# Optimization experiments

Measured on AMD Instinct MI355X. Metric: run time of the kernel, lower is better.

The kernel has to match this reference:

```python
import jax, jax.numpy as jnp
import numpy as np

NUM_ITEMS = 50000
IN_FEATS = 64
H_FEATS = 64
NUM_EDGES = 800000


def setup_inputs() -> dict:
    key = jax.random.key(0)
    ks = jax.random.split(key, 12)
    s_in = 1.0 / np.sqrt(IN_FEATS)
    s_h = 1.0 / np.sqrt(H_FEATS)
    return {
        "embed": jax.random.normal(ks[0], (NUM_ITEMS, IN_FEATS), jnp.float32),
        "W1_self": jax.random.normal(ks[1], (IN_FEATS, H_FEATS), jnp.float32) * s_in,
        "W1_neigh": jax.random.normal(ks[2], (IN_FEATS, H_FEATS), jnp.float32) * s_in,
        "b1": jax.random.normal(ks[3], (H_FEATS,), jnp.float32) * s_in,
        "W2_self": jax.random.normal(ks[4], (H_FEATS, H_FEATS), jnp.float32) * s_h,
        "W2_neigh": jax.random.normal(ks[5], (H_FEATS, H_FEATS), jnp.float32) * s_h,
        "b2": jax.random.normal(ks[6], (H_FEATS,), jnp.float32) * s_h,
        "W_fc": jax.random.normal(ks[7], (H_FEATS, IN_FEATS), jnp.float32) * s_h,
        "b_fc": jax.random.normal(ks[8], (IN_FEATS,), jnp.float32) * s_h,
        "item_ids": jnp.arange(NUM_ITEMS, dtype=jnp.int64),
        "src": jax.random.randint(ks[9], (NUM_EDGES,), 0, NUM_ITEMS, jnp.int64),
        "dst": jax.random.randint(ks[10], (NUM_EDGES,), 0, NUM_ITEMS, jnp.int64),
    }


def _sage_mean(h, src, dst, W_self, W_neigh, b, num_nodes):
    # gather src features along edges, mean-reduce into dst nodes
    agg = jax.ops.segment_sum(h[src], dst, num_segments=num_nodes)  # [N, d]
    deg = jax.ops.segment_sum(jnp.ones_like(dst, dtype=h.dtype), dst,
                              num_segments=num_nodes)
    h_neigh = agg / jnp.clip(deg, 1.0, None)[:, None]  # zero for isolated nodes
    return h @ W_self + h_neigh @ W_neigh + b


def reference(embed, W1_self, W1_neigh, b1, W2_self, W2_neigh, b2,
              W_fc, b_fc, item_ids, src, dst):
    n = embed.shape[0]
    x = embed[item_ids]                                   # embedding lookup [N, in]
    h = _sage_mean(x, src, dst, W1_self, W1_neigh, b1, n)  # SAGEConv 1
    h = jax.nn.relu(h)
    h = _sage_mean(h, src, dst, W2_self, W2_neigh, b2, n)  # SAGEConv 2
    return h @ W_fc + b_fc                                 # final linear
```

## Files before the change

### kernel.cpp

```cpp
#include <hip/hip_runtime.h>

#define NN 50000
#define NE 800000
#define F  64
#define CAP 64
#define NTILE 782
#define TPB   512

typedef float f32x4 __attribute__((ext_vector_type(4)));
typedef float f32x2 __attribute__((ext_vector_type(2)));

__device__ __forceinline__ unsigned bf16rne(float f) {
    unsigned u = __float_as_uint(f);
    return (u + 0x7fffu + ((u >> 16) & 1u)) >> 16;
}
__device__ __forceinline__ float bflo(unsigned p) { return __uint_as_float(p << 16); }
__device__ __forceinline__ float bfhi(unsigned p) { return __uint_as_float(p & 0xffff0000u); }
__device__ __forceinline__ f32x2 up2(unsigned p) {
    f32x2 r;
    r.x = __uint_as_float(p << 16);
    r.y = __uint_as_float(p & 0xffff0000u);
    return r;
}

__device__ __forceinline__ int nswz(int f, int n) { return f * 64 + (n ^ (((f >> 3) & 3) << 3)); }
__device__ __forceinline__ int aswz(int r, int n) { return r * 64 + (n ^ (((r >> 2) & 3) << 3)); }

__device__ __forceinline__ void add8(f32x2 s[4], const uint4 v) {
    s[0] += up2(v.x);
    s[1] += up2(v.y);
    s[2] += up2(v.z);
    s[3] += up2(v.w);
}


__launch_bounds__(256)
__global__ void k_build(const int* __restrict__ src, const int* __restrict__ dst,
                        int* __restrict__ cnt, unsigned short* __restrict__ csr,
                        const float* __restrict__ embed, const int* __restrict__ ids,
                        uint2* __restrict__ xb) {
    const int t = blockIdx.x * blockDim.x + threadIdx.x;
    if (t >= NE / 4) return;

    const int e0 = t * 4;
    const int4 d4 = *(const int4*)&dst[e0];
    const int4 s4 = *(const int4*)&src[e0];
    int sl0 = atomicAdd(&cnt[d4.x], 1) & (CAP - 1);
    int sl1 = atomicAdd(&cnt[d4.y], 1) & (CAP - 1);
    int sl2 = atomicAdd(&cnt[d4.z], 1) & (CAP - 1);
    int sl3 = atomicAdd(&cnt[d4.w], 1) & (CAP - 1);
    __builtin_nontemporal_store((unsigned short)s4.x, &csr[d4.x * CAP + sl0]);
    __builtin_nontemporal_store((unsigned short)s4.y, &csr[d4.y * CAP + sl1]);
    __builtin_nontemporal_store((unsigned short)s4.z, &csr[d4.z * CAP + sl2]);
    __builtin_nontemporal_store((unsigned short)s4.w, &csr[d4.w * CAP + sl3]);

    const int i  = t >> 2;
    const int c0 = (t & 3) * 4;
    const int rb = ids[i] * 16 + c0;
    float4 v0 = ((const float4*)embed)[rb + 0];
    float4 v1 = ((const float4*)embed)[rb + 1];
    float4 v2 = ((const float4*)embed)[rb + 2];
    float4 v3 = ((const float4*)embed)[rb + 3];
    uint4 p01, p23;
    p01.x = bf16rne(v0.x) | (bf16rne(v0.y) << 16);
    p01.y = bf16rne(v0.z) | (bf16rne(v0.w) << 16);
    p01.z = bf16rne(v1.x) | (bf16rne(v1.y) << 16);
    p01.w = bf16rne(v1.z) | (bf16rne(v1.w) << 16);
    p23.x = bf16rne(v2.x) | (bf16rne(v2.y) << 16);
    p23.y = bf16rne(v2.z) | (bf16rne(v2.w) << 16);
    p23.z = bf16rne(v3.x) | (bf16rne(v3.y) << 16);
    p23.w = bf16rne(v3.z) | (bf16rne(v3.w) << 16);
    uint4* xo = (uint4*)&xb[i * 16 + c0];
    xo[0] = p01;
    xo[1] = p23;
}


template <bool LAST>
__launch_bounds__(TPB)
__global__ void k_fused(const uint4* __restrict__ Ab, const int* __restrict__ cnt,
                        const unsigned short* __restrict__ csr,
                        const float* __restrict__ Ws, const float* __restrict__ Wn,
                        const float* __restrict__ b,
                        const float* __restrict__ Wfc, const float* __restrict__ bfc,
                        uint2* __restrict__ outb, float* __restrict__ out) {
    __shared__ alignas(16) float    NsT[F * 64];
    __shared__ alignas(16) unsigned Apk[32 * 64];
    __shared__ alignas(16) unsigned Wpk[F * F];

    const int tid = threadIdx.x;
    const int node0 = blockIdx.x * 64;

    for (int i = tid; i < F * F; i += TPB)
        Wpk[i] = bf16rne(Ws[i]) | (bf16rne(Wn[i]) << 16);

    {
        const int n = tid >> 3;
        const int c = tid & 7;
        const int lane = tid & 63;
        const int base = lane & 56;
        const int gnode = node0 + n;
        f32x2 s[4];
        s[0] = 0.f; s[1] = 0.f; s[2] = 0.f; s[3] = 0.f;
        uint4 a = make_uint4(0u, 0u, 0u, 0u);
        float inv = 0.f;
        if (gnode < NN) {
            a = Ab[gnode * 8 + c];
            int dc = cnt[gnode];
            int deg = dc < CAP ? dc : CAP;
            const int beg = gnode * CAP;
            int j = 0;
            for (; j + 8 <= deg; j += 8) {
                int v = (int)csr[beg + j + c];
                int i0 = __shfl(v, base + 0, 64), i1 = __shfl(v, base + 1, 64);
                int i2 = __shfl(v, base + 2, 64), i3 = __shfl(v, base + 3, 64);
                int i4 = __shfl(v, base + 4, 64), i5 = __shfl(v, base + 5, 64);
                int i6 = __shfl(v, base + 6, 64), i7 = __shfl(v, base + 7, 64);
                uint4 d0 = Ab[i0 * 8 + c], d1 = Ab[i1 * 8 + c];
                uint4 d2 = Ab[i2 * 8 + c], d3 = Ab[i3 * 8 + c];
                uint4 d4 = Ab[i4 * 8 + c], d5 = Ab[i5 * 8 + c];
                uint4 d6 = Ab[i6 * 8 + c], d7 = Ab[i7 * 8 + c];
                add8(s, d0); add8(s, d1); add8(s, d2); add8(s, d3);
                add8(s, d4); add8(s, d5); add8(s, d6); add8(s, d7);
            }
            int rem = deg - j;
            if (rem > 0) {
                int v = (int)csr[beg + j + (c < rem ? c : 0)];
                int idx[8];
#pragma unroll
                for (int k = 0; k < 8; ++k) idx[k] = __shfl(v, base + k, 64);
#pragma unroll
                for (int k = 0; k < 8; ++k)
                    if (k < rem) { uint4 d = Ab[idx[k] * 8 + c]; add8(s, d); }
            }
            inv = (deg > 0) ? 1.f / (float)deg : 0.f;
        }
        const int f = 8 * c;
        Apk[aswz(4 * c + 0, n)] = a.x;
        Apk[aswz(4 * c + 1, n)] = a.y;
        Apk[aswz(4 * c + 2, n)] = a.z;
        Apk[aswz(4 * c + 3, n)] = a.w;
#pragma unroll
        for (int q = 0; q < 4; ++q) {
            NsT[nswz(f + 2 * q + 0, n)] = s[q].x * inv;
            NsT[nswz(f + 2 * q + 1, n)] = s[q].y * inv;
        }
    }
    __syncthreads();

    const int tx = tid & 15, ty = tid >> 4;
    f32x2 acc[2][2];
    {
        f32x2 b01, b23;
        b01.x = b[4 * tx + 0]; b01.y = b[4 * tx + 1];
        b23.x = b[4 * tx + 2]; b23.y = b[4 * tx + 3];
        acc[0][0] = b01; acc[0][1] = b23;
        acc[1][0] = b01; acc[1][1] = b23;
    }
#pragma unroll 4
    for (int r = 0; r < 32; ++r) {
        const int k0 = 2 * r;
        uint2  ap = *(const uint2*)&Apk[aswz(r, 2 * ty)];
        float2 n0 = *(const float2*)&NsT[nswz(k0, 2 * ty)];
        float2 n1 = *(const float2*)&NsT[nswz(k0 + 1, 2 * ty)];
        uint4  w0 = *(const uint4*)&Wpk[k0 * 64 + 4 * tx];
        uint4  w1 = *(const uint4*)&Wpk[(k0 + 1) * 64 + 4 * tx];
        f32x2 ws0A, ws0B, wn0A, wn0B, ws1A, ws1B, wn1A, wn1B;
        ws0A.x = bflo(w0.x); ws0A.y = bflo(w0.y); ws0B.x = bflo(w0.z); ws0B.y = bflo(w0.w);
        wn0A.x = bfhi(w0.x); wn0A.y = bfhi(w0.y); wn0B.x = bfhi(w0.z); wn0B.y = bfhi(w0.w);
        ws1A.x = bflo(w1.x); ws1A.y = bflo(w1.y); ws1B.x = bflo(w1.z); ws1B.y = bflo(w1.w);
        wn1A.x = bfhi(w1.x); wn1A.y = bfhi(w1.y); wn1B.x = bfhi(w1.z); wn1B.y = bfhi(w1.w);
        const float a00 = bflo(ap.x), a01 = bfhi(ap.x);
        const float a10 = bflo(ap.y), a11 = bfhi(ap.y);
        acc[0][0] += a00 * ws0A + n0.x * wn0A;
        acc[0][1] += a00 * ws0B + n0.x * wn0B;
        acc[1][0] += a10 * ws0A + n0.y * wn0A;
        acc[1][1] += a10 * ws0B + n0.y * wn0B;
        acc[0][0] += a01 * ws1A + n1.x * wn1A;
        acc[0][1] += a01 * ws1B + n1.x * wn1B;
        acc[1][0] += a11 * ws1A + n1.y * wn1A;
        acc[1][1] += a11 * ws1B + n1.y * wn1B;
    }

    if (!LAST) {
#pragma unroll
        for (int i = 0; i < 2; ++i) {
            int node = node0 + 2 * ty + i;
            if (node < NN) {
                float o0 = acc[i][0].x > 0.f ? acc[i][0].x : 0.f;
                float o1 = acc[i][0].y > 0.f ? acc[i][0].y : 0.f;
                float o2 = acc[i][1].x > 0.f ? acc[i][1].x : 0.f;
                float o3 = acc[i][1].y > 0.f ? acc[i][1].y : 0.f;
                uint2 p;
                p.x = bf16rne(o0) | (bf16rne(o1) << 16);
                p.y = bf16rne(o2) | (bf16rne(o3) << 16);
                outb[node * 16 + tx] = p;
            }
        }
    } else {
        __syncthreads();
        float* Wf = (float*)Wpk;
#pragma unroll
        for (int i = 0; i < 2; ++i) {
            NsT[nswz(4 * tx + 0, 2 * ty + i)] = acc[i][0].x;
            NsT[nswz(4 * tx + 1, 2 * ty + i)] = acc[i][0].y;
            NsT[nswz(4 * tx + 2, 2 * ty + i)] = acc[i][1].x;
            NsT[nswz(4 * tx + 3, 2 * ty + i)] = acc[i][1].y;
        }
        for (int i = tid; i < F * F / 4; i += TPB)
            ((float4*)Wf)[i] = ((const float4*)Wfc)[i];
        __syncthreads();

        f32x2 acc2[2][2];
        {
            f32x2 b01, b23;
            b01.x = bfc[4 * tx + 0]; b01.y = bfc[4 * tx + 1];
            b23.x = bfc[4 * tx + 2]; b23.y = bfc[4 * tx + 3];
            acc2[0][0] = b01; acc2[0][1] = b23;
            acc2[1][0] = b01; acc2[1][1] = b23;
        }
#pragma unroll 4
        for (int k = 0; k < 64; ++k) {
            float2 a2 = *(const float2*)&NsT[nswz(k, 2 * ty)];
            float4 w4 = *(const float4*)&Wf[k * 64 + 4 * tx];
            f32x2 wA, wB;
            wA.x = w4.x; wA.y = w4.y; wB.x = w4.z; wB.y = w4.w;
            acc2[0][0] += a2.x * wA; acc2[0][1] += a2.x * wB;
            acc2[1][0] += a2.y * wA; acc2[1][1] += a2.y * wB;
        }
#pragma unroll
        for (int i = 0; i < 2; ++i) {
            int node = node0 + 2 * ty + i;
            if (node < NN) {
                f32x4 o;
                o.x = acc2[i][0].x; o.y = acc2[i][0].y;
                o.z = acc2[i][1].x; o.w = acc2[i][1].y;
                __builtin_nontemporal_store(o, (f32x4*)&out[node * 64 + 4 * tx]);
            }
        }
    }
}


extern "C" void kernel_launch(void* const* d_in, const int* in_sizes, int n_in,
                              void* d_out, int out_size, void* d_ws, size_t ws_size,
                              hipStream_t stream) {
    const float* embed = (const float*)d_in[0];
    const float* W1s = (const float*)d_in[1];
    const float* W1n = (const float*)d_in[2];
    const float* b1  = (const float*)d_in[3];
    const float* W2s = (const float*)d_in[4];
    const float* W2n = (const float*)d_in[5];
    const float* b2  = (const float*)d_in[6];
    const float* Wfc = (const float*)d_in[7];
    const float* bfc = (const float*)d_in[8];
    const int* ids = (const int*)d_in[9];
    const int* src = (const int*)d_in[10];
    const int* dst = (const int*)d_in[11];
    float* out = (float*)d_out;

    char* ws = (char*)d_ws;
    size_t off = 0;
    auto alloc = [&](size_t nb) {
        char* p = ws + off;
        off = (off + nb + 255) & ~(size_t)255;
        return p;
    };
    int*   cnt = (int*)alloc(NN * sizeof(int));
    size_t zero_bytes = off;
    unsigned short* csr = (unsigned short*)alloc((size_t)NN * CAP * sizeof(unsigned short));
    uint2* xb  = (uint2*)alloc((size_t)NN * 16 * sizeof(uint2));
    uint2* h1b = (uint2*)alloc((size_t)NN * 16 * sizeof(uint2));

    hipMemsetAsync(d_ws, 0, zero_bytes, stream);

    const int TB = 256;
    const int GB = (NE / 4 + TB - 1) / TB;
    k_build<<<GB, TB, 0, stream>>>(src, dst, cnt, csr, embed, ids, xb);

    k_fused<false><<<NTILE, TPB, 0, stream>>>((const uint4*)xb, cnt, csr,
                                              W1s, W1n, b1, nullptr, nullptr,
                                              h1b, nullptr);
    k_fused<true><<<NTILE, TPB, 0, stream>>>((const uint4*)h1b, cnt, csr,
                                             W2s, W2n, b2, Wfc, bfc,
                                             nullptr, out);
}
```

Before: 217.8 us.

## Split per-node neighbor lists into two source-range halves for gather locality

Neighbor slots for each destination node are split into two 32-entry buckets by whether the source index is in the lower or upper half of the node range, with separate counters. Aggregation walks the low-source bucket then the high-source bucket, so each pass of gathers hits a smaller region of the feature table and should reuse cache better. It also switches the index stores to normal stores and the index loads to nontemporal loads. In exchange there are twice as many counters to zero and read, more tail iterations per node, and a per-half cap of 32 that could drop edges for skewed degree distributions.

```diff
diff --git a/kernel.cpp b/kernel.cpp
--- a/kernel.cpp
+++ b/kernel.cpp
@@ -3,7 +3,8 @@
 #define NN 50000
 #define NE 800000
 #define F  64
-#define CAP 64
+#define HALF 25000
+#define HCAP 32
 #define NTILE 782
 #define TPB   512
 
@@ -45,14 +46,18 @@
     const int e0 = t * 4;
     const int4 d4 = *(const int4*)&dst[e0];
     const int4 s4 = *(const int4*)&src[e0];
-    int sl0 = atomicAdd(&cnt[d4.x], 1) & (CAP - 1);
-    int sl1 = atomicAdd(&cnt[d4.y], 1) & (CAP - 1);
-    int sl2 = atomicAdd(&cnt[d4.z], 1) & (CAP - 1);
-    int sl3 = atomicAdd(&cnt[d4.w], 1) & (CAP - 1);
-    __builtin_nontemporal_store((unsigned short)s4.x, &csr[d4.x * CAP + sl0]);
-    __builtin_nontemporal_store((unsigned short)s4.y, &csr[d4.y * CAP + sl1]);
-    __builtin_nontemporal_store((unsigned short)s4.z, &csr[d4.z * CAP + sl2]);
-    __builtin_nontemporal_store((unsigned short)s4.w, &csr[d4.w * CAP + sl3]);
+    const int h0 = (s4.x >= HALF) ? 1 : 0;
+    const int h1 = (s4.y >= HALF) ? 1 : 0;
+    const int h2 = (s4.z >= HALF) ? 1 : 0;
+    const int h3 = (s4.w >= HALF) ? 1 : 0;
+    int sl0 = atomicAdd(&cnt[d4.x * 2 + h0], 1) & (HCAP - 1);
+    int sl1 = atomicAdd(&cnt[d4.y * 2 + h1], 1) & (HCAP - 1);
+    int sl2 = atomicAdd(&cnt[d4.z * 2 + h2], 1) & (HCAP - 1);
+    int sl3 = atomicAdd(&cnt[d4.w * 2 + h3], 1) & (HCAP - 1);
+    csr[d4.x * 64 + h0 * HCAP + sl0] = (unsigned short)s4.x;
+    csr[d4.y * 64 + h1 * HCAP + sl1] = (unsigned short)s4.y;
+    csr[d4.z * 64 + h2 * HCAP + sl2] = (unsigned short)s4.z;
+    csr[d4.w * 64 + h3 * HCAP + sl3] = (unsigned short)s4.w;
 
     const int i  = t >> 2;
     const int c0 = (t & 3) * 4;
@@ -75,6 +80,36 @@
     xo[1] = p23;
 }
 
+__device__ __forceinline__ void agg_half(const uint4* __restrict__ Ab,
+                                         const unsigned short* __restrict__ csr,
+                                         int beg, int deg, int c, int base,
+                                         f32x2 s[4]) {
+    int j = 0;
+    for (; j + 8 <= deg; j += 8) {
+        int v = (int)__builtin_nontemporal_load(&csr[beg + j + c]);
+        int i0 = __shfl(v, base + 0, 64), i1 = __shfl(v, base + 1, 64);
+        int i2 = __shfl(v, base + 2, 64), i3 = __shfl(v, base + 3, 64);
+        int i4 = __shfl(v, base + 4, 64), i5 = __shfl(v, base + 5, 64);
+        int i6 = __shfl(v, base + 6, 64), i7 = __shfl(v, base + 7, 64);
+        uint4 d0 = Ab[i0 * 8 + c], d1 = Ab[i1 * 8 + c];
+        uint4 d2 = Ab[i2 * 8 + c], d3 = Ab[i3 * 8 + c];
+        uint4 d4 = Ab[i4 * 8 + c], d5 = Ab[i5 * 8 + c];
+        uint4 d6 = Ab[i6 * 8 + c], d7 = Ab[i7 * 8 + c];
+        add8(s, d0); add8(s, d1); add8(s, d2); add8(s, d3);
+        add8(s, d4); add8(s, d5); add8(s, d6); add8(s, d7);
+    }
+    int rem = deg - j;
+    if (rem > 0) {
+        int v = (int)__builtin_nontemporal_load(&csr[beg + j + (c < rem ? c : 0)]);
+        int idx[8];
+#pragma unroll
+        for (int k = 0; k < 8; ++k) idx[k] = __shfl(v, base + k, 64);
+#pragma unroll
+        for (int k = 0; k < 8; ++k)
+            if (k < rem) { uint4 d = Ab[idx[k] * 8 + c]; add8(s, d); }
+    }
+}
+
 
 template <bool LAST>
 __launch_bounds__(TPB)
@@ -106,33 +141,14 @@
         float inv = 0.f;
         if (gnode < NN) {
             a = Ab[gnode * 8 + c];
-            int dc = cnt[gnode];
-            int deg = dc < CAP ? dc : CAP;
-            const int beg = gnode * CAP;
-            int j = 0;
-            for (; j + 8 <= deg; j += 8) {
-                int v = (int)csr[beg + j + c];
-                int i0 = __shfl(v, base + 0, 64), i1 = __shfl(v, base + 1, 64);
-                int i2 = __shfl(v, base + 2, 64), i3 = __shfl(v, base + 3, 64);
-                int i4 = __shfl(v, base + 4, 64), i5 = __shfl(v, base + 5, 64);
-                int i6 = __shfl(v, base + 6, 64), i7 = __shfl(v, base + 7, 64);
-                uint4 d0 = Ab[i0 * 8 + c], d1 = Ab[i1 * 8 + c];
-                uint4 d2 = Ab[i2 * 8 + c], d3 = Ab[i3 * 8 + c];
-                uint4 d4 = Ab[i4 * 8 + c], d5 = Ab[i5 * 8 + c];
-                uint4 d6 = Ab[i6 * 8 + c], d7 = Ab[i7 * 8 + c];
-                add8(s, d0); add8(s, d1); add8(s, d2); add8(s, d3);
-                add8(s, d4); add8(s, d5); add8(s, d6); add8(s, d7);
-            }
-            int rem = deg - j;
-            if (rem > 0) {
-                int v = (int)csr[beg + j + (c < rem ? c : 0)];
-                int idx[8];
-#pragma unroll
-                for (int k = 0; k < 8; ++k) idx[k] = __shfl(v, base + k, 64);
-#pragma unroll
-                for (int k = 0; k < 8; ++k)
-                    if (k < rem) { uint4 d = Ab[idx[k] * 8 + c]; add8(s, d); }
-            }
+            int dlo = cnt[2 * gnode + 0];
+            int dhi = cnt[2 * gnode + 1];
+            dlo = dlo < HCAP ? dlo : HCAP;
+            dhi = dhi < HCAP ? dhi : HCAP;
+            const int beg = gnode * 64;
+            agg_half(Ab, csr, beg,        dlo, c, base, s);
+            agg_half(Ab, csr, beg + HCAP, dhi, c, base, s);
+            const int deg = dlo + dhi;
             inv = (deg > 0) ? 1.f / (float)deg : 0.f;
         }
         const int f = 8 * c;
@@ -266,9 +282,9 @@
         off = (off + nb + 255) & ~(size_t)255;
         return p;
     };
-    int*   cnt = (int*)alloc(NN * sizeof(int));
+    int*   cnt = (int*)alloc((size_t)NN * 2 * sizeof(int));
     size_t zero_bytes = off;
-    unsigned short* csr = (unsigned short*)alloc((size_t)NN * CAP * sizeof(unsigned short));
+    unsigned short* csr = (unsigned short*)alloc((size_t)NN * 64 * sizeof(unsigned short));
     uint2* xb  = (uint2*)alloc((size_t)NN * 16 * sizeof(uint2));
     uint2* h1b = (uint2*)alloc((size_t)NN * 16 * sizeof(uint2));
 
```

New measurement: 219.0 us. No clear change (+0.6%).

## Bin edges by destination tile, build per-tile CSR in shared memory

Applied to the files above, without the earlier changes.

Replaces the global per-node atomic CSR build with a two-level scheme. Edges are first appended to per-tile bins, split into 8 sub-bins by block class to spread atomic contention. The first fused layer kernel then builds each tile's 64-node adjacency in LDS with shared atomics, uses it directly, and writes it out for the second layer. This cuts scattered global atomics and 2-byte scattered stores, at the cost of an extra binlist buffer and an overflow risk if a sub-bin exceeds 256 edges.

```diff
diff --git a/kernel.cpp b/kernel.cpp
--- a/kernel.cpp
+++ b/kernel.cpp
@@ -6,6 +6,7 @@
 #define CAP 64
 #define NTILE 782
 #define TPB   512
+#define SBCAP 256
 
 typedef float f32x4 __attribute__((ext_vector_type(4)));
 typedef float f32x2 __attribute__((ext_vector_type(2)));
@@ -35,24 +36,26 @@
 
 
 __launch_bounds__(256)
-__global__ void k_build(const int* __restrict__ src, const int* __restrict__ dst,
-                        int* __restrict__ cnt, unsigned short* __restrict__ csr,
-                        const float* __restrict__ embed, const int* __restrict__ ids,
-                        uint2* __restrict__ xb) {
+__global__ void k_bin(const int* __restrict__ src, const int* __restrict__ dst,
+                      int* __restrict__ bincnt, unsigned* __restrict__ binlist,
+                      const float* __restrict__ embed, const int* __restrict__ ids,
+                      uint2* __restrict__ xb) {
     const int t = blockIdx.x * blockDim.x + threadIdx.x;
     if (t >= NE / 4) return;
+    const int cls = blockIdx.x & 7;
 
     const int e0 = t * 4;
     const int4 d4 = *(const int4*)&dst[e0];
     const int4 s4 = *(const int4*)&src[e0];
-    int sl0 = atomicAdd(&cnt[d4.x], 1) & (CAP - 1);
-    int sl1 = atomicAdd(&cnt[d4.y], 1) & (CAP - 1);
-    int sl2 = atomicAdd(&cnt[d4.z], 1) & (CAP - 1);
-    int sl3 = atomicAdd(&cnt[d4.w], 1) & (CAP - 1);
-    __builtin_nontemporal_store((unsigned short)s4.x, &csr[d4.x * CAP + sl0]);
-    __builtin_nontemporal_store((unsigned short)s4.y, &csr[d4.y * CAP + sl1]);
-    __builtin_nontemporal_store((unsigned short)s4.z, &csr[d4.z * CAP + sl2]);
-    __builtin_nontemporal_store((unsigned short)s4.w, &csr[d4.w * CAP + sl3]);
+#pragma unroll
+    for (int k = 0; k < 4; ++k) {
+        const int d = (k == 0) ? d4.x : (k == 1) ? d4.y : (k == 2) ? d4.z : d4.w;
+        const int s = (k == 0) ? s4.x : (k == 1) ? s4.y : (k == 2) ? s4.z : s4.w;
+        const int bin = (d >> 6) * 8 + cls;
+        int slot = atomicAdd(&bincnt[bin], 1);
+        if (slot < SBCAP)
+            binlist[bin * SBCAP + slot] = (unsigned)s | ((unsigned)(d & 63) << 16);
+    }
 
     const int i  = t >> 2;
     const int c0 = (t & 3) * 4;
@@ -76,10 +79,12 @@
 }
 
 
-template <bool LAST>
+template <bool FIRST>
 __launch_bounds__(TPB)
-__global__ void k_fused(const uint4* __restrict__ Ab, const int* __restrict__ cnt,
-                        const unsigned short* __restrict__ csr,
+__global__ void k_fused(const uint4* __restrict__ Ab,
+                        const int* __restrict__ cnt, const unsigned short* __restrict__ csr,
+                        const int* __restrict__ bincnt, const unsigned* __restrict__ binlist,
+                        unsigned short* __restrict__ csrg_out, int* __restrict__ cnt_out,
                         const float* __restrict__ Ws, const float* __restrict__ Wn,
                         const float* __restrict__ b,
                         const float* __restrict__ Wfc, const float* __restrict__ bfc,
@@ -87,12 +92,34 @@
     __shared__ alignas(16) float    NsT[F * 64];
     __shared__ alignas(16) unsigned Apk[32 * 64];
     __shared__ alignas(16) unsigned Wpk[F * F];
+    __shared__ alignas(16) unsigned short csrT[64 * 64];
+    __shared__ int lcnt[64];
 
     const int tid = threadIdx.x;
     const int node0 = blockIdx.x * 64;
 
     for (int i = tid; i < F * F; i += TPB)
         Wpk[i] = bf16rne(Ws[i]) | (bf16rne(Wn[i]) << 16);
+
+    if (FIRST) {
+        if (tid < 64) lcnt[tid] = 0;
+        __syncthreads();
+        const int tb8 = blockIdx.x * 8;
+#pragma unroll 1
+        for (int seg = 0; seg < 8; ++seg) {
+            int bc = bincnt[tb8 + seg];
+            if (bc > SBCAP) bc = SBCAP;
+            for (int e = tid; e < bc; e += TPB) {
+                unsigned u = binlist[(tb8 + seg) * SBCAP + e];
+                int n = (int)(u >> 16);
+                int s = atomicAdd(&lcnt[n], 1);
+                if (s < CAP) csrT[n * CAP + s] = (unsigned short)(u & 0xffffu);
+            }
+        }
+        __syncthreads();
+        ((uint4*)(csrg_out + (size_t)blockIdx.x * 4096))[tid] = ((const uint4*)csrT)[tid];
+        if (tid < 64 && node0 + tid < NN) cnt_out[node0 + tid] = lcnt[tid];
+    }
 
     {
         const int n = tid >> 3;
@@ -106,12 +133,12 @@
         float inv = 0.f;
         if (gnode < NN) {
             a = Ab[gnode * 8 + c];
-            int dc = cnt[gnode];
+            int dc = FIRST ? lcnt[n] : cnt[gnode];
             int deg = dc < CAP ? dc : CAP;
-            const int beg = gnode * CAP;
+            const unsigned short* row = FIRST ? &csrT[n * CAP] : &csr[(size_t)gnode * CAP];
             int j = 0;
             for (; j + 8 <= deg; j += 8) {
-                int v = (int)csr[beg + j + c];
+                int v = (int)row[j + c];
                 int i0 = __shfl(v, base + 0, 64), i1 = __shfl(v, base + 1, 64);
                 int i2 = __shfl(v, base + 2, 64), i3 = __shfl(v, base + 3, 64);
                 int i4 = __shfl(v, base + 4, 64), i5 = __shfl(v, base + 5, 64);
@@ -125,7 +152,7 @@
             }
             int rem = deg - j;
             if (rem > 0) {
-                int v = (int)csr[beg + j + (c < rem ? c : 0)];
+                int v = (int)row[j + (c < rem ? c : 0)];
                 int idx[8];
 #pragma unroll
                 for (int k = 0; k < 8; ++k) idx[k] = __shfl(v, base + k, 64);
@@ -182,7 +209,7 @@
         acc[1][1] += a11 * ws1B + n1.y * wn1B;
     }
 
-    if (!LAST) {
+    if (FIRST) {
 #pragma unroll
         for (int i = 0; i < 2; ++i) {
             int node = node0 + 2 * ty + i;
@@ -266,9 +293,11 @@
         off = (off + nb + 255) & ~(size_t)255;
         return p;
     };
+    int* bincnt = (int*)alloc((size_t)NTILE * 8 * sizeof(int));
+    size_t zero_bytes = off;
+    unsigned* binlist = (unsigned*)alloc((size_t)NTILE * 8 * SBCAP * sizeof(unsigned));
+    unsigned short* csrg = (unsigned short*)alloc((size_t)NTILE * 64 * CAP * sizeof(unsigned short));
     int*   cnt = (int*)alloc(NN * sizeof(int));
-    size_t zero_bytes = off;
-    unsigned short* csr = (unsigned short*)alloc((size_t)NN * CAP * sizeof(unsigned short));
     uint2* xb  = (uint2*)alloc((size_t)NN * 16 * sizeof(uint2));
     uint2* h1b = (uint2*)alloc((size_t)NN * 16 * sizeof(uint2));
 
@@ -276,12 +305,16 @@
 
     const int TB = 256;
     const int GB = (NE / 4 + TB - 1) / TB;
-    k_build<<<GB, TB, 0, stream>>>(src, dst, cnt, csr, embed, ids, xb);
-
-    k_fused<false><<<NTILE, TPB, 0, stream>>>((const uint4*)xb, cnt, csr,
-                                              W1s, W1n, b1, nullptr, nullptr,
-                                              h1b, nullptr);
-    k_fused<true><<<NTILE, TPB, 0, stream>>>((const uint4*)h1b, cnt, csr,
-                                             W2s, W2n, b2, Wfc, bfc,
-                                             nullptr, out);
-}
+    k_bin<<<GB, TB, 0, stream>>>(src, dst, bincnt, binlist, embed, ids, xb);
+
+    k_fused<true><<<NTILE, TPB, 0, stream>>>((const uint4*)xb,
+                                             nullptr, nullptr,
+                                             bincnt, binlist, csrg, cnt,
+                                             W1s, W1n, b1, nullptr, nullptr,
+                                             h1b, nullptr);
+    k_fused<false><<<NTILE, TPB, 0, stream>>>((const uint4*)h1b,
+                                              cnt, csrg,
+                                              nullptr, nullptr, nullptr, nullptr,
+                                              W2s, W2n, b2, Wfc, bfc,
+                                              nullptr, out);
+}
```

Result: no change. 220.8 us (+1.4%).
